# Optimization experiments

Measured on AMD Instinct MI355X. Metric: run time of the kernel, lower is better.

## Reference

```python
import jax, jax.numpy as jnp
import numpy as np

N_NODES, N_EDGES, D_IN, D_HID, D_OUT = 100000, 3200000, 512, 64, 64


def _gcn_conv(x, W, b, src, dst, n_nodes):
    """PyG-style GCNConv: x' = D^{-1/2} A_hat D^{-1/2} (x W) + b, self-loops already in (src,dst)."""
    h = x @ W  # [N, F_out]
    deg = jax.ops.segment_sum(jnp.ones_like(dst, dtype=h.dtype), dst, num_segments=n_nodes)
    dinv = jax.lax.rsqrt(deg)  # deg >= 1 because self-loops are included
    norm = dinv[src] * dinv[dst]  # [E]
    msg = h[src] * norm[:, None]  # gather + scale, [E, F_out]
    return jax.ops.segment_sum(msg, dst, num_segments=n_nodes) + b


def setup_inputs() -> dict:
    key = jax.random.key(0)
    ks = jax.random.split(key, 8)
    x = jax.random.normal(ks[0], (N_NODES, D_IN), dtype=jnp.float32)
    edge_index = jax.random.randint(ks[1], (2, N_EDGES), 0, N_NODES, dtype=jnp.int32)
    W1 = jax.random.normal(ks[2], (D_IN, D_HID), dtype=jnp.float32) * (1.0 / np.sqrt(D_IN))
    b1 = jnp.zeros((D_HID,), dtype=jnp.float32)
    W2 = jax.random.normal(ks[3], (D_HID, D_OUT), dtype=jnp.float32) * (1.0 / np.sqrt(D_HID))
    b2 = jnp.zeros((D_OUT,), dtype=jnp.float32)
    Wlin = jax.random.normal(ks[4], (D_HID, D_OUT), dtype=jnp.float32) * (1.0 / np.sqrt(D_HID))
    blin = jnp.zeros((D_OUT,), dtype=jnp.float32)
    return {"x": x, "edge_index": edge_index, "W1": W1, "b1": b1,
            "W2": W2, "b2": b2, "Wlin": Wlin, "blin": blin}


def reference(x, edge_index, W1, b1, W2, b2, Wlin, blin):
    n = x.shape[0]
    loops = jnp.arange(n, dtype=edge_index.dtype)
    src = jnp.concatenate([edge_index[0], loops])
    dst = jnp.concatenate([edge_index[1], loops])
    h = _gcn_conv(x, W1, b1, src, dst, n)
    h = jax.nn.relu(h)
    h = _gcn_conv(h, W2, b2, src, dst, n)
    return h @ Wlin + blin
```

## Files before the change

### kernel.cpp

```cpp
#include <hip/hip_runtime.h>

#define DIN 512
#define DH  64
#define BKT_SHIFT 10
#define BKT_NODES 1024
#define MAXBKT 128
#define TILE 8192
#define SRC_BITS 17
#define SRC_MASK ((1u << SRC_BITS) - 1)

typedef __attribute__((ext_vector_type(8))) _Float16 half8_t;
typedef __attribute__((ext_vector_type(4))) float float4_t;

__global__ __launch_bounds__(256) void k_prep(const float* __restrict__ W1,
                                              const float* __restrict__ W2,
                                              const float* __restrict__ b2,
                                              const float* __restrict__ Wlin,
                                              const float* __restrict__ blin,
                                              _Float16* __restrict__ Wt,
                                              _Float16* __restrict__ Wct,
                                              float* __restrict__ bias_out,
                                              int* __restrict__ gcur,
                                              int nbkt, int cap) {
  const int tid = threadIdx.x;
  if (blockIdx.x == 0) {
    __shared__ float WcS[64 * 64];
    for (int idx = tid; idx < 64 * 64; idx += 256) {
      int i = idx >> 6, j = idx & 63;
      float s = 0.f;
      #pragma unroll 8
      for (int k = 0; k < 64; ++k) s = fmaf(W2[i * 64 + k], Wlin[k * 64 + j], s);
      WcS[idx] = s;
    }
    if (tid < 64) {
      float s = blin[tid];
      #pragma unroll 8
      for (int k = 0; k < 64; ++k) s = fmaf(b2[k], Wlin[k * 64 + tid], s);
      bias_out[tid] = s;
    }
    for (int b = tid; b < nbkt; b += 256) gcur[b] = b * cap;
    __syncthreads();
    for (int G = tid; G < 64 * 64 / 8; G += 256) {
      int n = G >> 3, k = (G & 7) * 8;
      half8_t h;
      #pragma unroll
      for (int j = 0; j < 8; ++j) h[j] = (_Float16)WcS[(k + j) * 64 + n];
      *(half8_t*)&Wct[(size_t)n * 64 + k] = h;
    }
  } else {
    __shared__ _Float16 T[64][136];
    const int k0 = (blockIdx.x - 1) * 128;
    for (int idx = tid; idx < 128 * 64; idx += 256) {
      int kk = idx >> 6, n = idx & 63;
      T[n][kk] = (_Float16)W1[(size_t)(k0 + kk) * 64 + n];
    }
    __syncthreads();
    for (int G = tid; G < 64 * 16; G += 256) {
      int n = G >> 4, g = (G & 15) * 8;
      half8_t h = *(const half8_t*)&T[n][g];
      *(half8_t*)&Wt[(size_t)n * 512 + k0 + g] = h;
    }
  }
}

__global__ __launch_bounds__(256) void k_bin(const int* __restrict__ src,
                                             const int* __restrict__ dst, int n_edges,
                                             int* __restrict__ gcur,
                                             unsigned int* __restrict__ tmp,
                                             int nbkt, int cap) {
  __shared__ int cnt[MAXBKT];
  __shared__ int base[MAXBKT];
  int t = threadIdx.x;
  for (int b = t; b < nbkt; b += 256) cnt[b] = 0;
  __syncthreads();
  int e0 = blockIdx.x * TILE;
  int e1 = min(e0 + TILE, n_edges);
  for (int e = e0 + t; e < e1; e += 256)
    atomicAdd(&cnt[dst[e] >> BKT_SHIFT], 1);
  __syncthreads();
  for (int b = t; b < nbkt; b += 256) {
    int c = cnt[b];
    base[b] = c ? atomicAdd(&gcur[b], c) : 0;
    cnt[b] = 0;
  }
  __syncthreads();
  for (int e = e0 + t; e < e1; e += 256) {
    int d = dst[e];
    int bkt = d >> BKT_SHIFT;
    int off = atomicAdd(&cnt[bkt], 1);
    int pos = base[bkt] + off;
    if (pos < (bkt + 1) * cap)
      tmp[pos] = (unsigned int)src[e] | ((unsigned int)(d & (BKT_NODES - 1)) << SRC_BITS);
  }
}

__global__ __launch_bounds__(256) void k_place(const unsigned int* __restrict__ tmp,
                                               const int* __restrict__ gcur,
                                               int* __restrict__ rowbeg,
                                               int* __restrict__ rowcnt,
                                               float* __restrict__ dinv,
                                               int* __restrict__ srcs,
                                               int n_nodes, int cap) {
  __shared__ int cnt[BKT_NODES];
  __shared__ int sh[256];
  const int t = threadIdx.x;
  const int bkt = blockIdx.x;
  #pragma unroll
  for (int k = 0; k < BKT_NODES / 256; ++k) cnt[t + 256 * k] = 0;
  __syncthreads();
  const int beg = bkt * cap;
  const int end = min(gcur[bkt], (bkt + 1) * cap);
  for (int j = beg + t; j < end; j += 256)
    atomicAdd(&cnt[tmp[j] >> SRC_BITS], 1);
  __syncthreads();
  int v[4];
  int s = 0;
  const int base = t * 4;
  #pragma unroll
  for (int k = 0; k < 4; ++k) {
    v[k] = cnt[base + k];
    s += v[k];
  }
  sh[t] = s;
  __syncthreads();
  for (int off = 1; off < 256; off <<= 1) {
    int x = sh[t];
    int y = (t >= off) ? sh[t - off] : 0;
    __syncthreads();
    sh[t] = x + y;
    __syncthreads();
  }
  int excl = sh[t] - s;
  #pragma unroll
  for (int k = 0; k < 4; ++k) {
    int idx = base + k;
    int node = (bkt << BKT_SHIFT) + idx;
    if (node < n_nodes) {
      rowbeg[node] = beg + excl;
      rowcnt[node] = v[k];
      dinv[node] = rsqrtf((float)(v[k] + 1));
    }
    cnt[idx] = excl;
    excl += v[k];
  }
  __syncthreads();
  for (int j = beg + t; j < end; j += 256) {
    unsigned int e = tmp[j];
    int r = e >> SRC_BITS;
    int pos = atomicAdd(&cnt[r], 1);
    srcs[beg + pos] = (int)(e & SRC_MASK);
  }
}

template <int KDIM, bool A_HALF>
__global__ __launch_bounds__(1024) void k_mfma(const void* __restrict__ Ain,
                                               const _Float16* __restrict__ Bt,
                                               _Float16* __restrict__ Ch, int M) {
  constexpr int BS_HALVES = (64 * KDIM > 16384) ? 64 * KDIM : 16384;
  __shared__ _Float16 Bs[BS_HALVES];
  const int tid = threadIdx.x;
  for (int G = tid; G < 8 * KDIM; G += 1024) {
    int n = G / (KDIM / 8);
    int g = G % (KDIM / 8);
    half8_t h = *(const half8_t*)&Bt[(size_t)G * 8];
    *(half8_t*)&Bs[n * KDIM + ((g ^ (n & 7)) * 8)] = h;
  }
  __syncthreads();

  const int wave = tid >> 6, lane = tid & 63;
  const int quad = lane >> 4, lrow = lane & 15;
  const int row = blockIdx.x * 256 + wave * 16 + lrow;
  const int rowc = min(row, M - 1);

  float4_t acc[4] = {{0.f, 0.f, 0.f, 0.f}, {0.f, 0.f, 0.f, 0.f},
                     {0.f, 0.f, 0.f, 0.f}, {0.f, 0.f, 0.f, 0.f}};

  #pragma unroll
  for (int k0 = 0; k0 < KDIM; k0 += 32) {
    half8_t a;
    if (A_HALF) {
      a = *(const half8_t*)((const _Float16*)Ain + (size_t)rowc * KDIM + k0 + quad * 8);
    } else {
      const float* Af = (const float*)Ain + (size_t)rowc * KDIM + k0 + quad * 8;
      float4 x0 = *(const float4*)Af;
      float4 x1 = *(const float4*)(Af + 4);
      a[0] = (_Float16)x0.x; a[1] = (_Float16)x0.y;
      a[2] = (_Float16)x0.z; a[3] = (_Float16)x0.w;
      a[4] = (_Float16)x1.x; a[5] = (_Float16)x1.y;
      a[6] = (_Float16)x1.z; a[7] = (_Float16)x1.w;
    }
    const int g = (k0 >> 3) + quad;
    #pragma unroll
    for (int nb = 0; nb < 4; ++nb) {
      int n = nb * 16 + lrow;
      half8_t b = *(const half8_t*)&Bs[n * KDIM + ((g ^ (n & 7)) * 8)];
      acc[nb] = __builtin_amdgcn_mfma_f32_16x16x32_f16(a, b, acc[nb], 0, 0, 0);
    }
  }

  __syncthreads();
  _Float16* scratch = Bs + wave * 1024;
  #pragma unroll
  for (int nb = 0; nb < 4; ++nb)
    #pragma unroll
    for (int r = 0; r < 4; ++r)
      scratch[(quad * 4 + r) * 64 + nb * 16 + lrow] = (_Float16)acc[nb][r];
  const int r2 = lane >> 2, c2 = (lane & 3) * 16;
  const int row_out = blockIdx.x * 256 + wave * 16 + r2;
  half8_t o0 = *(const half8_t*)&scratch[r2 * 64 + c2];
  half8_t o1 = *(const half8_t*)&scratch[r2 * 64 + c2 + 8];
  if (row_out < M) {
    *(half8_t*)&Ch[(size_t)row_out * 64 + c2] = o0;
    *(half8_t*)&Ch[(size_t)row_out * 64 + c2 + 8] = o1;
  }
}

__global__ __launch_bounds__(256) void k_gather(const _Float16* __restrict__ feath,
                                                const int* __restrict__ rowbeg,
                                                const int* __restrict__ rowcnt,
                                                const int* __restrict__ srcs,
                                                const float* __restrict__ dinv,
                                                const float* __restrict__ bias,
                                                _Float16* __restrict__ outh,
                                                float* __restrict__ outf,
                                                int n_nodes) {
  int node = blockIdx.x * 4 + (threadIdx.x >> 6);
  int lane = threadIdx.x & 63;
  if (node >= n_nodes) return;
  const int esub = lane >> 3;
  const int ch8 = (lane & 7) * 8;
  const int beg = rowbeg[node];
  const int end = beg + rowcnt[node];
  float acc[8] = {0.f, 0.f, 0.f, 0.f, 0.f, 0.f, 0.f, 0.f};
  int j = beg;
  for (; j + 16 <= end; j += 16) {
    int s0 = srcs[j + esub];
    int s1 = srcs[j + 8 + esub];
    float w0 = dinv[s0], w1 = dinv[s1];
    half8_t f0 = *(const half8_t*)&feath[(size_t)s0 * 64 + ch8];
    half8_t f1 = *(const half8_t*)&feath[(size_t)s1 * 64 + ch8];
    #pragma unroll
    for (int k = 0; k < 8; ++k) acc[k] = fmaf((float)f0[k], w0, acc[k]);
    #pragma unroll
    for (int k = 0; k < 8; ++k) acc[k] = fmaf((float)f1[k], w1, acc[k]);
  }
  for (; j < end; j += 8) {
    int idx = j + esub;
    bool act = idx < end;
    int s = srcs[act ? idx : beg];
    float w = act ? dinv[s] : 0.f;
    half8_t f = *(const half8_t*)&feath[(size_t)s * 64 + ch8];
    #pragma unroll
    for (int k = 0; k < 8; ++k) acc[k] = fmaf((float)f[k], w, acc[k]);
  }
  #pragma unroll
  for (int m = 8; m <= 32; m <<= 1)
    #pragma unroll
    for (int k = 0; k < 8; ++k) acc[k] += __shfl_xor(acc[k], m, 64);
  if (esub == 0) {
    float dn = dinv[node];
    half8_t sf = *(const half8_t*)&feath[(size_t)node * 64 + ch8];
    float v[8];
    #pragma unroll
    for (int k = 0; k < 8; ++k)
      v[k] = fmaf(fmaf((float)sf[k], dn, acc[k]), dn, bias[ch8 + k]);
    if (outh) {
      half8_t o;
      #pragma unroll
      for (int k = 0; k < 8; ++k) o[k] = (_Float16)fmaxf(v[k], 0.f);
      *(half8_t*)&outh[(size_t)node * 64 + ch8] = o;
    } else {
      float4 o0 = make_float4(v[0], v[1], v[2], v[3]);
      float4 o1 = make_float4(v[4], v[5], v[6], v[7]);
      *(float4*)&outf[(size_t)node * 64 + ch8] = o0;
      *(float4*)&outf[(size_t)node * 64 + ch8 + 4] = o1;
    }
  }
}

extern "C" void kernel_launch(void* const* d_in, const int* in_sizes, int n_in,
                              void* d_out, int out_size, void* d_ws, size_t ws_size,
                              hipStream_t stream) {
  const float* x    = (const float*)d_in[0];
  const int*   ei   = (const int*)d_in[1];
  const float* W1   = (const float*)d_in[2];
  const float* b1   = (const float*)d_in[3];
  const float* W2   = (const float*)d_in[4];
  const float* b2   = (const float*)d_in[5];
  const float* Wlin = (const float*)d_in[6];
  const float* blin = (const float*)d_in[7];
  float* out = (float*)d_out;

  const int n_nodes = in_sizes[0] / DIN;
  const int n_edges = in_sizes[1] / 2;
  const int* src = ei;
  const int* dst = ei + n_edges;
  const int nbkt = (n_nodes + BKT_NODES - 1) >> BKT_SHIFT;
  const int ntiles = (n_edges + TILE - 1) / TILE;
  const int cap = ((n_edges / nbkt) * 5 / 4 + 1024 + 255) & ~255;

  char* ws = (char*)d_ws;
  size_t off = 0;
  auto alloc = [&](size_t bytes) {
    void* p = ws + off;
    off += (bytes + 255) & ~(size_t)255;
    return p;
  };
  const size_t featH = (size_t)n_nodes * DH * 2;
  const size_t padE = (size_t)nbkt * cap;
  _Float16*     feath1   = (_Float16*)alloc(featH);
  _Float16*     h1r      = (_Float16*)alloc(featH);
  _Float16*     feath2   = (_Float16*)alloc(featH);
  unsigned int* tmp      = (unsigned int*)alloc(padE * 4);
  int*          srcs     = (int*)alloc(padE * 4);
  float*        dinv     = (float*)alloc((size_t)n_nodes * 4);
  int*          rowbeg   = (int*)alloc((size_t)n_nodes * 4);
  int*          rowcnt   = (int*)alloc((size_t)n_nodes * 4);
  int*          gcur     = (int*)alloc((size_t)MAXBKT * 4);
  _Float16*     Wt       = (_Float16*)alloc(64 * 512 * 2);
  _Float16*     Wct      = (_Float16*)alloc(64 * 64 * 2);
  float*        bias_out = (float*)alloc(64 * 4);

  k_prep<<<5, 256, 0, stream>>>(W1, W2, b2, Wlin, blin, Wt, Wct, bias_out,
                                gcur, nbkt, cap);
  k_bin<<<ntiles, 256, 0, stream>>>(src, dst, n_edges, gcur, tmp, nbkt, cap);
  k_place<<<nbkt, 256, 0, stream>>>(tmp, gcur, rowbeg, rowcnt, dinv, srcs,
                                    n_nodes, cap);

  const int mblocks = (n_nodes + 255) / 256;
  const int agblocks = (n_nodes + 3) / 4;

  k_mfma<512, false><<<mblocks, 1024, 0, stream>>>(x, Wt, feath1, n_nodes);
  k_gather<<<agblocks, 256, 0, stream>>>(feath1, rowbeg, rowcnt, srcs, dinv, b1,
                                         h1r, nullptr, n_nodes);

  k_mfma<64, true><<<mblocks, 1024, 0, stream>>>(h1r, Wct, feath2, n_nodes);
  k_gather<<<agblocks, 256, 0, stream>>>(feath2, rowbeg, rowcnt, srcs, dinv,
                                         bias_out, nullptr, out, n_nodes);
}
```

Baseline: 598.9 us.

## Pre-scale GEMM outputs by source dinv and merge prep with binning kernel

The GEMM epilogue now multiplies each output row by dinv of that node, so the gather kernel sums pre-scaled features and no longer does a random dinv[src] lookup per edge. The prep and edge-binning kernels are merged into one launch, with gcur zeroed by a memset and bucket offsets made relative. This removes one random 4-byte gather per edge in each aggregation pass and one kernel launch. In exchange the GEMM now reads dinv, which makes it depend on k_place, and fp16 rounding now happens after the scaling.

```diff
diff --git a/kernel.cpp b/kernel.cpp
--- a/kernel.cpp
+++ b/kernel.cpp
@@ -12,16 +12,20 @@
 typedef __attribute__((ext_vector_type(8))) _Float16 half8_t;
 typedef __attribute__((ext_vector_type(4))) float float4_t;
 
-__global__ __launch_bounds__(256) void k_prep(const float* __restrict__ W1,
-                                              const float* __restrict__ W2,
-                                              const float* __restrict__ b2,
-                                              const float* __restrict__ Wlin,
-                                              const float* __restrict__ blin,
-                                              _Float16* __restrict__ Wt,
-                                              _Float16* __restrict__ Wct,
-                                              float* __restrict__ bias_out,
-                                              int* __restrict__ gcur,
-                                              int nbkt, int cap) {
+__global__ __launch_bounds__(256) void k_prepbin(const float* __restrict__ W1,
+                                                 const float* __restrict__ W2,
+                                                 const float* __restrict__ b2,
+                                                 const float* __restrict__ Wlin,
+                                                 const float* __restrict__ blin,
+                                                 _Float16* __restrict__ Wt,
+                                                 _Float16* __restrict__ Wct,
+                                                 float* __restrict__ bias_out,
+                                                 const int* __restrict__ src,
+                                                 const int* __restrict__ dst,
+                                                 int n_edges,
+                                                 int* __restrict__ gcur,
+                                                 unsigned int* __restrict__ tmp,
+                                                 int nbkt, int cap) {
   const int tid = threadIdx.x;
   if (blockIdx.x == 0) {
     __shared__ float WcS[64 * 64];
@@ -38,7 +42,6 @@
       for (int k = 0; k < 64; ++k) s = fmaf(b2[k], Wlin[k * 64 + tid], s);
       bias_out[tid] = s;
     }
-    for (int b = tid; b < nbkt; b += 256) gcur[b] = b * cap;
     __syncthreads();
     for (int G = tid; G < 64 * 64 / 8; G += 256) {
       int n = G >> 3, k = (G & 7) * 8;
@@ -47,7 +50,7 @@
       for (int j = 0; j < 8; ++j) h[j] = (_Float16)WcS[(k + j) * 64 + n];
       *(half8_t*)&Wct[(size_t)n * 64 + k] = h;
     }
-  } else {
+  } else if (blockIdx.x <= 4) {
     __shared__ _Float16 T[64][136];
     const int k0 = (blockIdx.x - 1) * 128;
     for (int idx = tid; idx < 128 * 64; idx += 256) {
@@ -60,37 +63,31 @@
       half8_t h = *(const half8_t*)&T[n][g];
       *(half8_t*)&Wt[(size_t)n * 512 + k0 + g] = h;
     }
-  }
-}
-
-__global__ __launch_bounds__(256) void k_bin(const int* __restrict__ src,
-                                             const int* __restrict__ dst, int n_edges,
-                                             int* __restrict__ gcur,
-                                             unsigned int* __restrict__ tmp,
-                                             int nbkt, int cap) {
-  __shared__ int cnt[MAXBKT];
-  __shared__ int base[MAXBKT];
-  int t = threadIdx.x;
-  for (int b = t; b < nbkt; b += 256) cnt[b] = 0;
-  __syncthreads();
-  int e0 = blockIdx.x * TILE;
-  int e1 = min(e0 + TILE, n_edges);
-  for (int e = e0 + t; e < e1; e += 256)
-    atomicAdd(&cnt[dst[e] >> BKT_SHIFT], 1);
-  __syncthreads();
-  for (int b = t; b < nbkt; b += 256) {
-    int c = cnt[b];
-    base[b] = c ? atomicAdd(&gcur[b], c) : 0;
-    cnt[b] = 0;
-  }
-  __syncthreads();
-  for (int e = e0 + t; e < e1; e += 256) {
-    int d = dst[e];
-    int bkt = d >> BKT_SHIFT;
-    int off = atomicAdd(&cnt[bkt], 1);
-    int pos = base[bkt] + off;
-    if (pos < (bkt + 1) * cap)
-      tmp[pos] = (unsigned int)src[e] | ((unsigned int)(d & (BKT_NODES - 1)) << SRC_BITS);
+  } else {
+    __shared__ int cnt[MAXBKT];
+    __shared__ int base[MAXBKT];
+    for (int b = tid; b < nbkt; b += 256) cnt[b] = 0;
+    __syncthreads();
+    int e0 = (blockIdx.x - 5) * TILE;
+    int e1 = min(e0 + TILE, n_edges);
+    for (int e = e0 + tid; e < e1; e += 256)
+      atomicAdd(&cnt[dst[e] >> BKT_SHIFT], 1);
+    __syncthreads();
+    for (int b = tid; b < nbkt; b += 256) {
+      int c = cnt[b];
+      base[b] = c ? (b * cap + atomicAdd(&gcur[b], c)) : 0;
+      cnt[b] = 0;
+    }
+    __syncthreads();
+    for (int e = e0 + tid; e < e1; e += 256) {
+      int d = dst[e];
+      int bkt = d >> BKT_SHIFT;
+      int off = atomicAdd(&cnt[bkt], 1);
+      int pos = base[bkt] + off;
+      if (pos < (bkt + 1) * cap)
+        tmp[pos] = (unsigned int)src[e] |
+                   ((unsigned int)(d & (BKT_NODES - 1)) << SRC_BITS);
+    }
   }
 }
 
@@ -109,7 +106,7 @@
   for (int k = 0; k < BKT_NODES / 256; ++k) cnt[t + 256 * k] = 0;
   __syncthreads();
   const int beg = bkt * cap;
-  const int end = min(gcur[bkt], (bkt + 1) * cap);
+  const int end = beg + min(gcur[bkt], cap);
   for (int j = beg + t; j < end; j += 256)
     atomicAdd(&cnt[tmp[j] >> SRC_BITS], 1);
   __syncthreads();
@@ -155,6 +152,7 @@
 template <int KDIM, bool A_HALF>
 __global__ __launch_bounds__(1024) void k_mfma(const void* __restrict__ Ain,
                                                const _Float16* __restrict__ Bt,
+                                               const float* __restrict__ dinv,
                                                _Float16* __restrict__ Ch, int M) {
   constexpr int BS_HALVES = (64 * KDIM > 16384) ? 64 * KDIM : 16384;
   __shared__ _Float16 Bs[BS_HALVES];
@@ -198,13 +196,18 @@
     }
   }
 
+  const int orow_base = blockIdx.x * 256 + wave * 16 + quad * 4;
+  float dnr[4];
+  #pragma unroll
+  for (int r = 0; r < 4; ++r) dnr[r] = dinv[min(orow_base + r, M - 1)];
+
   __syncthreads();
   _Float16* scratch = Bs + wave * 1024;
   #pragma unroll
   for (int nb = 0; nb < 4; ++nb)
     #pragma unroll
     for (int r = 0; r < 4; ++r)
-      scratch[(quad * 4 + r) * 64 + nb * 16 + lrow] = (_Float16)acc[nb][r];
+      scratch[(quad * 4 + r) * 64 + nb * 16 + lrow] = (_Float16)(acc[nb][r] * dnr[r]);
   const int r2 = lane >> 2, c2 = (lane & 3) * 16;
   const int row_out = blockIdx.x * 256 + wave * 16 + r2;
   half8_t o0 = *(const half8_t*)&scratch[r2 * 64 + c2];
@@ -215,7 +218,7 @@
   }
 }
 
-__global__ __launch_bounds__(256) void k_gather(const _Float16* __restrict__ feath,
+__global__ __launch_bounds__(256) void k_gather(const _Float16* __restrict__ fs,
                                                 const int* __restrict__ rowbeg,
                                                 const int* __restrict__ rowcnt,
                                                 const int* __restrict__ srcs,
@@ -236,20 +239,19 @@
   for (; j + 16 <= end; j += 16) {
     int s0 = srcs[j + esub];
     int s1 = srcs[j + 8 + esub];
-    float w0 = dinv[s0], w1 = dinv[s1];
-    half8_t f0 = *(const half8_t*)&feath[(size_t)s0 * 64 + ch8];
-    half8_t f1 = *(const half8_t*)&feath[(size_t)s1 * 64 + ch8];
-    #pragma unroll
-    for (int k = 0; k < 8; ++k) acc[k] = fmaf((float)f0[k], w0, acc[k]);
-    #pragma unroll
-    for (int k = 0; k < 8; ++k) acc[k] = fmaf((float)f1[k], w1, acc[k]);
+    half8_t f0 = *(const half8_t*)&fs[(size_t)s0 * 64 + ch8];
+    half8_t f1 = *(const half8_t*)&fs[(size_t)s1 * 64 + ch8];
+    #pragma unroll
+    for (int k = 0; k < 8; ++k) acc[k] += (float)f0[k];
+    #pragma unroll
+    for (int k = 0; k < 8; ++k) acc[k] += (float)f1[k];
   }
   for (; j < end; j += 8) {
     int idx = j + esub;
     bool act = idx < end;
     int s = srcs[act ? idx : beg];
-    float w = act ? dinv[s] : 0.f;
-    half8_t f = *(const half8_t*)&feath[(size_t)s * 64 + ch8];
+    float w = act ? 1.f : 0.f;
+    half8_t f = *(const half8_t*)&fs[(size_t)s * 64 + ch8];
     #pragma unroll
     for (int k = 0; k < 8; ++k) acc[k] = fmaf((float)f[k], w, acc[k]);
   }
@@ -259,11 +261,11 @@
     for (int k = 0; k < 8; ++k) acc[k] += __shfl_xor(acc[k], m, 64);
   if (esub == 0) {
     float dn = dinv[node];
-    half8_t sf = *(const half8_t*)&feath[(size_t)node * 64 + ch8];
+    half8_t sf = *(const half8_t*)&fs[(size_t)node * 64 + ch8];
     float v[8];
     #pragma unroll
     for (int k = 0; k < 8; ++k)
-      v[k] = fmaf(fmaf((float)sf[k], dn, acc[k]), dn, bias[ch8 + k]);
+      v[k] = fmaf(acc[k] + (float)sf[k], dn, bias[ch8 + k]);
     if (outh) {
       half8_t o;
       #pragma unroll
@@ -308,9 +310,9 @@
   };
   const size_t featH = (size_t)n_nodes * DH * 2;
   const size_t padE = (size_t)nbkt * cap;
-  _Float16*     feath1   = (_Float16*)alloc(featH);
+  _Float16*     fs1      = (_Float16*)alloc(featH);
   _Float16*     h1r      = (_Float16*)alloc(featH);
-  _Float16*     feath2   = (_Float16*)alloc(featH);
+  _Float16*     fs2      = (_Float16*)alloc(featH);
   unsigned int* tmp      = (unsigned int*)alloc(padE * 4);
   int*          srcs     = (int*)alloc(padE * 4);
   float*        dinv     = (float*)alloc((size_t)n_nodes * 4);
@@ -321,20 +323,22 @@
   _Float16*     Wct      = (_Float16*)alloc(64 * 64 * 2);
   float*        bias_out = (float*)alloc(64 * 4);
 
-  k_prep<<<5, 256, 0, stream>>>(W1, W2, b2, Wlin, blin, Wt, Wct, bias_out,
-                                gcur, nbkt, cap);
-  k_bin<<<ntiles, 256, 0, stream>>>(src, dst, n_edges, gcur, tmp, nbkt, cap);
+  hipMemsetAsync(gcur, 0, (size_t)nbkt * 4, stream);
+
+  k_prepbin<<<5 + ntiles, 256, 0, stream>>>(W1, W2, b2, Wlin, blin, Wt, Wct,
+                                            bias_out, src, dst, n_edges, gcur,
+                                            tmp, nbkt, cap);
   k_place<<<nbkt, 256, 0, stream>>>(tmp, gcur, rowbeg, rowcnt, dinv, srcs,
                                     n_nodes, cap);
 
   const int mblocks = (n_nodes + 255) / 256;
   const int agblocks = (n_nodes + 3) / 4;
 
-  k_mfma<512, false><<<mblocks, 1024, 0, stream>>>(x, Wt, feath1, n_nodes);
-  k_gather<<<agblocks, 256, 0, stream>>>(feath1, rowbeg, rowcnt, srcs, dinv, b1,
+  k_mfma<512, false><<<mblocks, 1024, 0, stream>>>(x, Wt, dinv, fs1, n_nodes);
+  k_gather<<<agblocks, 256, 0, stream>>>(fs1, rowbeg, rowcnt, srcs, dinv, b1,
                                          h1r, nullptr, n_nodes);
 
-  k_mfma<64, true><<<mblocks, 1024, 0, stream>>>(h1r, Wct, feath2, n_nodes);
-  k_gather<<<agblocks, 256, 0, stream>>>(feath2, rowbeg, rowcnt, srcs, dinv,
+  k_mfma<64, true><<<mblocks, 1024, 0, stream>>>(h1r, Wct, dinv, fs2, n_nodes);
+  k_gather<<<agblocks, 256, 0, stream>>>(fs2, rowbeg, rowcnt, srcs, dinv,
                                          bias_out, nullptr, out, n_nodes);
 }
```

Measured after the change: 570.9 us. -4.7%, faster.
